# Performance work log

Hardware: AMD Instinct MI355X
Metric: run time of the kernel (lower is better)

## Reference

```python
import jax, jax.numpy as jnp
import numpy as np

B, S, MW = 128, 256, 21          # batch, sentence length, max word length
VOCAB, E_CHAR, E_WORD, K = 100, 50, 256, 5


def setup_inputs() -> dict:
    key = jax.random.key(0)
    ks = jax.random.split(key, 6)
    padded_sents = jax.random.randint(ks[0], (B, S, MW), 0, VOCAB)
    emb_table = jax.random.normal(ks[1], (VOCAB, E_CHAR), jnp.float32) * 0.1
    emb_table = emb_table.at[0].set(0.0)  # pad_token_idx row zeroed (padding_idx)
    conv_w = jax.random.normal(ks[2], (E_WORD, E_CHAR, K), jnp.float32) * 0.05
    conv_b = jnp.zeros((E_WORD,), jnp.float32)
    w_proj = jax.random.normal(ks[3], (E_WORD, E_WORD), jnp.float32) * 0.05
    b_proj = jnp.zeros((E_WORD,), jnp.float32)
    w_gate = jax.random.normal(ks[4], (E_WORD, E_WORD), jnp.float32) * 0.05
    b_gate = jnp.zeros((E_WORD,), jnp.float32)
    return {
        "padded_sents": padded_sents,
        "emb_table": emb_table,
        "conv_w": conv_w,
        "conv_b": conv_b,
        "w_proj": w_proj,
        "b_proj": b_proj,
        "w_gate": w_gate,
        "b_gate": b_gate,
    }


def reference(padded_sents, emb_table, conv_w, conv_b, w_proj, b_proj, w_gate, b_gate):
    b, s, mw = padded_sents.shape
    # char embedding lookup: [B,S,MW,E_CHAR]
    x = emb_table[padded_sents]
    # fold (B,S) into one batch dim and move channels first: [B*S, E_CHAR, MW]
    x = x.reshape(b * s, mw, -1).transpose(0, 2, 1)
    # Conv1d VALID over char positions: [B*S, E_WORD, MW-K+1]
    y = jax.lax.conv_general_dilated(
        x, conv_w, window_strides=(1,), padding="VALID",
        dimension_numbers=("NCH", "OIH", "NCH"))
    y = jax.nn.relu(y + conv_b[None, :, None])
    # max-pool over remaining char positions: [B*S, E_WORD]
    y = jnp.max(y, axis=2)
    # Highway network
    proj = jax.nn.relu(y @ w_proj.T + b_proj)
    gate = jax.nn.sigmoid(y @ w_gate.T + b_gate)
    out = gate * proj + (1.0 - gate) * y
    # dropout in eval mode (identity)
    return out.reshape(b, s, -1)
```

## Files before the change

### kernel.cpp

```cpp
#include <hip/hip_runtime.h>

#define B_     128
#define S_     256
#define MW_    21
#define VOCAB_ 100
#define EC_    50
#define EW_    256
#define KW_    5
#define T_     17
#define NW_    (B_ * S_)
#define GROWS  (VOCAB_ * KW_)
#define WPB    128
#define P1B    200

typedef _Float16 f16x8 __attribute__((ext_vector_type(8)));
typedef float    f32x4 __attribute__((ext_vector_type(4)));

__global__ __launch_bounds__(256) void k_prep(const float* __restrict__ emb,
                                              const float* __restrict__ cw,
                                              const float* __restrict__ Wp,
                                              const float* __restrict__ Wg,
                                              _Float16* __restrict__ g,
                                              _Float16* __restrict__ wpf,
                                              _Float16* __restrict__ wgf) {
  const int bi = blockIdx.x;
  if (bi < P1B) {
    __shared__ float ls[64 * 250];
    const int vp = bi >> 2, ot = bi & 3;
    const int o0 = ot * 64;
    const int tid = threadIdx.x;
    const float4* __restrict__ cw4 = (const float4*)cw + ot * 4000;
#pragma unroll 4
    for (int idx4 = tid; idx4 < 4000; idx4 += 256)
      *(float4*)&ls[idx4 * 4] = cw4[idx4];
    __syncthreads();

    const int l = tid & 63, wv = tid >> 6;
#pragma unroll
    for (int vv = 0; vv < 2; ++vv) {
      const int v = vp * 2 + vv;
      const float* __restrict__ er = emb + v * EC_;
      float acc = 0.f;
#pragma unroll
      for (int i = 0; i < EC_; ++i)
        acc += er[i] * ls[l * 250 + i * KW_ + wv];
      g[(v * KW_ + wv) * EW_ + o0 + l] = (_Float16)acc;
      if (wv == 0) {
        float a4 = 0.f;
#pragma unroll
        for (int i = 0; i < EC_; ++i)
          a4 += er[i] * ls[l * 250 + i * KW_ + 4];
        g[(v * KW_ + 4) * EW_ + o0 + l] = (_Float16)a4;
      }
    }
  } else {
    const int fl  = (bi - P1B) * 256 + threadIdx.x;
    const int nt  = fl >> 9;
    const int rem = fl & 511;
    const int ks  = rem >> 6;
    const int l   = rem & 63;
    const int n   = nt * 16 + (l & 15);
    const int kc  = ks * 32 + (l >> 4) * 8;
    const int src = n * EW_ + kc;
    const float4 p0 = *(const float4*)&Wp[src], p1 = *(const float4*)&Wp[src + 4];
    const float4 q0 = *(const float4*)&Wg[src], q1 = *(const float4*)&Wg[src + 4];
    f16x8 hp = {(_Float16)p0.x, (_Float16)p0.y, (_Float16)p0.z, (_Float16)p0.w,
                (_Float16)p1.x, (_Float16)p1.y, (_Float16)p1.z, (_Float16)p1.w};
    f16x8 hg = {(_Float16)q0.x, (_Float16)q0.y, (_Float16)q0.z, (_Float16)q0.w,
                (_Float16)q1.x, (_Float16)q1.y, (_Float16)q1.z, (_Float16)q1.w};
    *(f16x8*)&wpf[fl * 8] = hp;
    *(f16x8*)&wgf[fl * 8] = hg;
  }
}

__global__ __launch_bounds__(512, 2) void k_mega(const int* __restrict__ idx,
                                                 const _Float16* __restrict__ g,
                                                 const float* __restrict__ cb,
                                                 const _Float16* __restrict__ wpf,
                                                 const _Float16* __restrict__ wgf,
                                                 const float* __restrict__ bp,
                                                 const float* __restrict__ bg,
                                                 float* __restrict__ out) {
  __shared__ __align__(16) _Float16 lds[32768 + GROWS * 64];
  _Float16* y_s = lds;
  _Float16* g_s = lds + 32768;

  const int tid  = threadIdx.x;
  const int wave = tid >> 6, lane = tid & 63;
  const int m0 = blockIdx.x * WPB;
  const int wq = lane >> 3, og = lane & 7;

#pragma unroll
  for (int i = 0; i < 8; ++i) {
    const int c = tid + i * 512;
    if (c < GROWS * 8) {
      const int row = c >> 3, cc = c & 7;
      *(f16x8*)&g_s[row * 64 + cc * 8] = *(const f16x8*)&g[row * EW_ + cc * 8];
    }
  }
  __syncthreads();

  f16x8 pre[8];
#pragma unroll
  for (int chunk = 0; chunk < 4; ++chunk) {
    const int oc0 = chunk * 64;
    if (chunk < 3) {
#pragma unroll
      for (int i = 0; i < 8; ++i) {
        const int c = tid + i * 512;
        if (c < GROWS * 8) {
          const int row = c >> 3, cc = c & 7;
          pre[i] = *(const f16x8*)&g[row * EW_ + oc0 + 64 + cc * 8];
        }
      }
    }

    f16x8 bias;
#pragma unroll
    for (int j = 0; j < 8; ++j) bias[j] = (_Float16)cb[oc0 + og * 8 + j];

    const int ks_w    = chunk * 2 + (og >> 2);
    const int lane_hi = (og & 3) << 4;

#pragma unroll
    for (int it = 0; it < 2; ++it) {
      const int wl = it * 64 + wave * 8 + wq;
      const int* __restrict__ ip = idx + (m0 + wl) * MW_;
      int base[MW_];
#pragma unroll
      for (int c = 0; c < MW_; ++c)
        base[c] = ip[c] * (KW_ * 64) + og * 8;

      const _Float16 NEG = (_Float16)(-60000.0f);
      f16x8 mx = {NEG, NEG, NEG, NEG, NEG, NEG, NEG, NEG};
#pragma unroll
      for (int t = 0; t < T_; ++t) {
        f16x8 s = *(const f16x8*)&g_s[base[t]];
#pragma unroll
        for (int k = 1; k < KW_; ++k)
          s += *(const f16x8*)&g_s[base[t + k] + k * 64];
        mx = __builtin_elementwise_max(mx, s);
      }
      const f16x8 zero8 = {0, 0, 0, 0, 0, 0, 0, 0};
      mx = __builtin_elementwise_max(mx + bias, zero8);

      const int mt = wl >> 4;
      const int lt = ((wl & 15) | lane_hi) ^ og;
      *(f16x8*)&y_s[((mt * 8 + ks_w) * 64 + lt) * 8] = mx;
    }
    __syncthreads();
    if (chunk < 3) {
#pragma unroll
      for (int i = 0; i < 8; ++i) {
        const int c = tid + i * 512;
        if (c < GROWS * 8) {
          const int row = c >> 3, cc = c & 7;
          *(f16x8*)&g_s[row * 64 + cc * 8] = pre[i];
        }
      }
      __syncthreads();
    }
  }

  const int mtp2 = wave >> 2, nq = wave & 3;
  const int quad = lane >> 4, r16 = lane & 15;

  const f32x4 zero = {0.f, 0.f, 0.f, 0.f};
  f32x4 accp[4][4], accg[4][4];
#pragma unroll
  for (int mi = 0; mi < 4; ++mi)
#pragma unroll
    for (int nf = 0; nf < 4; ++nf) { accp[mi][nf] = zero; accg[mi][nf] = zero; }

#pragma unroll
  for (int ks = 0; ks < 8; ++ks) {
    const int key = ((ks & 1) << 2) | quad;
    f16x8 a[4];
#pragma unroll
    for (int mi = 0; mi < 4; ++mi)
      a[mi] = *(const f16x8*)&y_s[(((mtp2 * 4 + mi) * 8 + ks) * 64 + (lane ^ key)) * 8];
#pragma unroll
    for (int nf = 0; nf < 4; ++nf) {
      const int nt = nq * 4 + nf;
      const int off = ((nt * 8 + ks) * 64 + lane) * 8;
      const f16x8 bpv = *(const f16x8*)&wpf[off];
      const f16x8 bgv = *(const f16x8*)&wgf[off];
#pragma unroll
      for (int mi = 0; mi < 4; ++mi) {
        accp[mi][nf] = __builtin_amdgcn_mfma_f32_16x16x32_f16(a[mi], bpv, accp[mi][nf], 0, 0, 0);
        accg[mi][nf] = __builtin_amdgcn_mfma_f32_16x16x32_f16(a[mi], bgv, accg[mi][nf], 0, 0, 0);
      }
    }
  }

#pragma unroll
  for (int mi = 0; mi < 4; ++mi) {
    const int mt = mtp2 * 4 + mi;
#pragma unroll
    for (int nf = 0; nf < 4; ++nf) {
      const int n = nq * 64 + nf * 16 + r16;
      const float bpn = bp[n];
      const float bgn = bg[n];
      const int ks_e = n >> 5;
      const int lane_e = ((n >> 3) & 3) << 4;
      const int og_e = (n >> 3) & 7;
      const int je = n & 7;
#pragma unroll
      for (int reg = 0; reg < 4; ++reg) {
        const int m = mt * 16 + quad * 4 + reg;
        float p = fmaxf(accp[mi][nf][reg] + bpn, 0.f);
        const float gz = accg[mi][nf][reg] + bgn;
        const float gate = 1.f / (1.f + __expf(-gz));
        const float yv =
            (float)y_s[((mt * 8 + ks_e) * 64 + (((m & 15) | lane_e) ^ og_e)) * 8 + je];
        out[(m0 + m) * EW_ + n] = gate * p + (1.f - gate) * yv;
      }
    }
  }
}

extern "C" void kernel_launch(void* const* d_in, const int* in_sizes, int n_in,
                              void* d_out, int out_size, void* d_ws, size_t ws_size,
                              hipStream_t stream) {
  (void)in_sizes; (void)n_in; (void)out_size; (void)ws_size;
  const int*   idx = (const int*)d_in[0];
  const float* emb = (const float*)d_in[1];
  const float* cw  = (const float*)d_in[2];
  const float* cb  = (const float*)d_in[3];
  const float* wp  = (const float*)d_in[4];
  const float* bpp = (const float*)d_in[5];
  const float* wgt = (const float*)d_in[6];
  const float* bgg = (const float*)d_in[7];
  float* out = (float*)d_out;
  _Float16* g_ws = (_Float16*)d_ws;
  _Float16* wp_f = g_ws + GROWS * EW_;
  _Float16* wg_f = wp_f + EW_ * EW_;

  k_prep<<<P1B + 32, 256, 0, stream>>>(emb, cw, wp, wgt, g_ws, wp_f, wg_f);
  k_mega<<<NW_ / WPB, 512, 0, stream>>>(idx, g_ws, cb, wp_f, wg_f, bpp, bgg, out);
}
```

Baseline: 120.3 us.

## Warp-specialize mega kernel: conv waves overlap with MFMA highway waves per chunk

Halves words per block to 64 and splits the 8 waves into 4 conv waves and 4 GEMM waves. The GEMM waves consume each finished 64-channel chunk of y while the conv waves compute the next chunk, so the gather/max conv and the MFMA highway run concurrently instead of in sequence. Char index bases are hoisted into registers once per word. In exchange only half the waves do conv work, the block count doubles so the g table is reloaded twice as often, and register pressure in the specialized waves goes up.

```diff
diff --git a/kernel.cpp b/kernel.cpp
--- a/kernel.cpp
+++ b/kernel.cpp
@@ -10,7 +10,7 @@
 #define T_     17
 #define NW_    (B_ * S_)
 #define GROWS  (VOCAB_ * KW_)
-#define WPB    128
+#define WPB    64
 #define P1B    200
 
 typedef _Float16 f16x8 __attribute__((ext_vector_type(8)));
@@ -81,9 +81,9 @@
                                                  const float* __restrict__ bp,
                                                  const float* __restrict__ bg,
                                                  float* __restrict__ out) {
-  __shared__ __align__(16) _Float16 lds[32768 + GROWS * 64];
+  __shared__ __align__(16) _Float16 lds[16384 + GROWS * 64];
   _Float16* y_s = lds;
-  _Float16* g_s = lds + 32768;
+  _Float16* g_s = lds + 16384;
 
   const int tid  = threadIdx.x;
   const int wave = tid >> 6, lane = tid & 63;
@@ -100,6 +100,31 @@
   }
   __syncthreads();
 
+  const bool isConv = wave < 4;
+  const int quad = lane >> 4, r16 = lane & 15;
+  const int nq = wave & 3;
+
+  int base[2][MW_];
+  if (isConv) {
+#pragma unroll
+    for (int it = 0; it < 2; ++it) {
+      const int wl = it * 32 + wave * 8 + wq;
+      const int* __restrict__ ip = idx + (m0 + wl) * MW_;
+#pragma unroll
+      for (int c = 0; c < MW_; ++c)
+        base[it][c] = ip[c] * (KW_ * 64) + og * 8;
+    }
+  }
+
+  f32x4 accp[4][4], accg[4][4];
+  if (!isConv) {
+    const f32x4 zero = {0.f, 0.f, 0.f, 0.f};
+#pragma unroll
+    for (int mi = 0; mi < 4; ++mi)
+#pragma unroll
+      for (int nf = 0; nf < 4; ++nf) { accp[mi][nf] = zero; accg[mi][nf] = zero; }
+  }
+
   f16x8 pre[8];
 #pragma unroll
   for (int chunk = 0; chunk < 4; ++chunk) {
@@ -115,38 +140,53 @@
       }
     }
 
-    f16x8 bias;
-#pragma unroll
-    for (int j = 0; j < 8; ++j) bias[j] = (_Float16)cb[oc0 + og * 8 + j];
-
-    const int ks_w    = chunk * 2 + (og >> 2);
-    const int lane_hi = (og & 3) << 4;
-
-#pragma unroll
-    for (int it = 0; it < 2; ++it) {
-      const int wl = it * 64 + wave * 8 + wq;
-      const int* __restrict__ ip = idx + (m0 + wl) * MW_;
-      int base[MW_];
-#pragma unroll
-      for (int c = 0; c < MW_; ++c)
-        base[c] = ip[c] * (KW_ * 64) + og * 8;
-
-      const _Float16 NEG = (_Float16)(-60000.0f);
-      f16x8 mx = {NEG, NEG, NEG, NEG, NEG, NEG, NEG, NEG};
-#pragma unroll
-      for (int t = 0; t < T_; ++t) {
-        f16x8 s = *(const f16x8*)&g_s[base[t]];
-#pragma unroll
-        for (int k = 1; k < KW_; ++k)
-          s += *(const f16x8*)&g_s[base[t + k] + k * 64];
-        mx = __builtin_elementwise_max(mx, s);
-      }
-      const f16x8 zero8 = {0, 0, 0, 0, 0, 0, 0, 0};
-      mx = __builtin_elementwise_max(mx + bias, zero8);
-
-      const int mt = wl >> 4;
-      const int lt = ((wl & 15) | lane_hi) ^ og;
-      *(f16x8*)&y_s[((mt * 8 + ks_w) * 64 + lt) * 8] = mx;
+    if (isConv) {
+      f16x8 bias;
+#pragma unroll
+      for (int j = 0; j < 8; ++j) bias[j] = (_Float16)cb[oc0 + og * 8 + j];
+      const int ks_w    = chunk * 2 + (og >> 2);
+      const int lane_hi = (og & 3) << 4;
+#pragma unroll
+      for (int it = 0; it < 2; ++it) {
+        const int wl = it * 32 + wave * 8 + wq;
+        const _Float16 NEG = (_Float16)(-60000.0f);
+        f16x8 mx = {NEG, NEG, NEG, NEG, NEG, NEG, NEG, NEG};
+#pragma unroll
+        for (int t = 0; t < T_; ++t) {
+          f16x8 s = *(const f16x8*)&g_s[base[it][t]];
+#pragma unroll
+          for (int k = 1; k < KW_; ++k)
+            s += *(const f16x8*)&g_s[base[it][t + k] + k * 64];
+          mx = __builtin_elementwise_max(mx, s);
+        }
+        const f16x8 zero8 = {0, 0, 0, 0, 0, 0, 0, 0};
+        mx = __builtin_elementwise_max(mx + bias, zero8);
+        const int mt = wl >> 4;
+        const int lt = ((wl & 15) | lane_hi) ^ og;
+        *(f16x8*)&y_s[((mt * 8 + ks_w) * 64 + lt) * 8] = mx;
+      }
+    } else if (chunk > 0) {
+#pragma unroll
+      for (int ks2 = 0; ks2 < 2; ++ks2) {
+        const int ks = (chunk - 1) * 2 + ks2;
+        const int key = ((ks & 1) << 2) | quad;
+        f16x8 a[4];
+#pragma unroll
+        for (int mi = 0; mi < 4; ++mi)
+          a[mi] = *(const f16x8*)&y_s[((mi * 8 + ks) * 64 + (lane ^ key)) * 8];
+#pragma unroll
+        for (int nf = 0; nf < 4; ++nf) {
+          const int nt = nq * 4 + nf;
+          const int off = ((nt * 8 + ks) * 64 + lane) * 8;
+          const f16x8 bpv = *(const f16x8*)&wpf[off];
+          const f16x8 bgv = *(const f16x8*)&wgf[off];
+#pragma unroll
+          for (int mi = 0; mi < 4; ++mi) {
+            accp[mi][nf] = __builtin_amdgcn_mfma_f32_16x16x32_f16(a[mi], bpv, accp[mi][nf], 0, 0, 0);
+            accg[mi][nf] = __builtin_amdgcn_mfma_f32_16x16x32_f16(a[mi], bgv, accg[mi][nf], 0, 0, 0);
+          }
+        }
+      }
     }
     __syncthreads();
     if (chunk < 3) {
@@ -162,58 +202,50 @@
     }
   }
 
-  const int mtp2 = wave >> 2, nq = wave & 3;
-  const int quad = lane >> 4, r16 = lane & 15;
-
-  const f32x4 zero = {0.f, 0.f, 0.f, 0.f};
-  f32x4 accp[4][4], accg[4][4];
-#pragma unroll
-  for (int mi = 0; mi < 4; ++mi)
-#pragma unroll
-    for (int nf = 0; nf < 4; ++nf) { accp[mi][nf] = zero; accg[mi][nf] = zero; }
-
-#pragma unroll
-  for (int ks = 0; ks < 8; ++ks) {
-    const int key = ((ks & 1) << 2) | quad;
-    f16x8 a[4];
-#pragma unroll
-    for (int mi = 0; mi < 4; ++mi)
-      a[mi] = *(const f16x8*)&y_s[(((mtp2 * 4 + mi) * 8 + ks) * 64 + (lane ^ key)) * 8];
-#pragma unroll
-    for (int nf = 0; nf < 4; ++nf) {
-      const int nt = nq * 4 + nf;
-      const int off = ((nt * 8 + ks) * 64 + lane) * 8;
-      const f16x8 bpv = *(const f16x8*)&wpf[off];
-      const f16x8 bgv = *(const f16x8*)&wgf[off];
-#pragma unroll
-      for (int mi = 0; mi < 4; ++mi) {
-        accp[mi][nf] = __builtin_amdgcn_mfma_f32_16x16x32_f16(a[mi], bpv, accp[mi][nf], 0, 0, 0);
-        accg[mi][nf] = __builtin_amdgcn_mfma_f32_16x16x32_f16(a[mi], bgv, accg[mi][nf], 0, 0, 0);
-      }
-    }
-  }
-
-#pragma unroll
-  for (int mi = 0; mi < 4; ++mi) {
-    const int mt = mtp2 * 4 + mi;
-#pragma unroll
-    for (int nf = 0; nf < 4; ++nf) {
-      const int n = nq * 64 + nf * 16 + r16;
-      const float bpn = bp[n];
-      const float bgn = bg[n];
-      const int ks_e = n >> 5;
-      const int lane_e = ((n >> 3) & 3) << 4;
-      const int og_e = (n >> 3) & 7;
-      const int je = n & 7;
-#pragma unroll
-      for (int reg = 0; reg < 4; ++reg) {
-        const int m = mt * 16 + quad * 4 + reg;
-        float p = fmaxf(accp[mi][nf][reg] + bpn, 0.f);
-        const float gz = accg[mi][nf][reg] + bgn;
-        const float gate = 1.f / (1.f + __expf(-gz));
-        const float yv =
-            (float)y_s[((mt * 8 + ks_e) * 64 + (((m & 15) | lane_e) ^ og_e)) * 8 + je];
-        out[(m0 + m) * EW_ + n] = gate * p + (1.f - gate) * yv;
+  if (!isConv) {
+#pragma unroll
+    for (int ks2 = 0; ks2 < 2; ++ks2) {
+      const int ks = 6 + ks2;
+      const int key = ((ks & 1) << 2) | quad;
+      f16x8 a[4];
+#pragma unroll
+      for (int mi = 0; mi < 4; ++mi)
+        a[mi] = *(const f16x8*)&y_s[((mi * 8 + ks) * 64 + (lane ^ key)) * 8];
+#pragma unroll
+      for (int nf = 0; nf < 4; ++nf) {
+        const int nt = nq * 4 + nf;
+        const int off = ((nt * 8 + ks) * 64 + lane) * 8;
+        const f16x8 bpv = *(const f16x8*)&wpf[off];
+        const f16x8 bgv = *(const f16x8*)&wgf[off];
+#pragma unroll
+        for (int mi = 0; mi < 4; ++mi) {
+          accp[mi][nf] = __builtin_amdgcn_mfma_f32_16x16x32_f16(a[mi], bpv, accp[mi][nf], 0, 0, 0);
+          accg[mi][nf] = __builtin_amdgcn_mfma_f32_16x16x32_f16(a[mi], bgv, accg[mi][nf], 0, 0, 0);
+        }
+      }
+    }
+
+#pragma unroll
+    for (int mi = 0; mi < 4; ++mi) {
+#pragma unroll
+      for (int nf = 0; nf < 4; ++nf) {
+        const int n = nq * 64 + nf * 16 + r16;
+        const float bpn = bp[n];
+        const float bgn = bg[n];
+        const int ks_e = n >> 5;
+        const int lane_e = ((n >> 3) & 3) << 4;
+        const int og_e = (n >> 3) & 7;
+        const int je = n & 7;
+#pragma unroll
+        for (int reg = 0; reg < 4; ++reg) {
+          const int m = mi * 16 + quad * 4 + reg;
+          float p = fmaxf(accp[mi][nf][reg] + bpn, 0.f);
+          const float gz = accg[mi][nf][reg] + bgn;
+          const float gate = 1.f / (1.f + __expf(-gz));
+          const float yv =
+              (float)y_s[((mi * 8 + ks_e) * 64 + (((m & 15) | lane_e) ^ og_e)) * 8 + je];
+          out[(m0 + m) * EW_ + n] = gate * p + (1.f - gate) * yv;
+        }
       }
     }
   }
```

Result: slower. 155.4 us (+29.1%).

## Halve words per block and stream conv table in 32-channel chunks

Applied to the files above, without the earlier changes.

Blocks now handle 64 words with 256 threads instead of 128 words with 512 threads. The gathered conv table is staged through LDS in 32-channel slices over 8 chunks rather than 64-channel slices over 4, which roughly halves LDS per block and lets more blocks fit per CU. Each thread now keeps one word's character indices for the whole kernel instead of reloading them every chunk, and the y tile swizzle is changed to a rotation. The cost is twice as many chunk iterations and barriers per block, and every block re-reads the weight matrices for half as many rows.

```diff
diff --git a/kernel.cpp b/kernel.cpp
--- a/kernel.cpp
+++ b/kernel.cpp
@@ -10,7 +10,8 @@
 #define T_     17
 #define NW_    (B_ * S_)
 #define GROWS  (VOCAB_ * KW_)
-#define WPB    128
+#define WPB    64
+#define CCH    32
 #define P1B    200
 
 typedef _Float16 f16x8 __attribute__((ext_vector_type(8)));
@@ -73,7 +74,7 @@
   }
 }
 
-__global__ __launch_bounds__(512, 2) void k_mega(const int* __restrict__ idx,
+__global__ __launch_bounds__(256, 2) void k_mega(const int* __restrict__ idx,
                                                  const _Float16* __restrict__ g,
                                                  const float* __restrict__ cb,
                                                  const _Float16* __restrict__ wpf,
@@ -81,36 +82,45 @@
                                                  const float* __restrict__ bp,
                                                  const float* __restrict__ bg,
                                                  float* __restrict__ out) {
-  __shared__ __align__(16) _Float16 lds[32768 + GROWS * 64];
+  __shared__ __align__(16) _Float16 lds[16384 + GROWS * CCH];
   _Float16* y_s = lds;
-  _Float16* g_s = lds + 32768;
+  _Float16* g_s = lds + 16384;
 
   const int tid  = threadIdx.x;
   const int wave = tid >> 6, lane = tid & 63;
   const int m0 = blockIdx.x * WPB;
-  const int wq = lane >> 3, og = lane & 7;
+  const int w  = tid >> 2;
+  const int og = tid & 3;
 
 #pragma unroll
   for (int i = 0; i < 8; ++i) {
-    const int c = tid + i * 512;
-    if (c < GROWS * 8) {
-      const int row = c >> 3, cc = c & 7;
-      *(f16x8*)&g_s[row * 64 + cc * 8] = *(const f16x8*)&g[row * EW_ + cc * 8];
+    const int c = tid + i * 256;
+    if (c < GROWS * 4) {
+      const int row = c >> 2, cc = c & 3;
+      *(f16x8*)&g_s[row * CCH + cc * 8] = *(const f16x8*)&g[row * EW_ + cc * 8];
     }
   }
   __syncthreads();
 
+  const int* __restrict__ ipr = idx + (m0 + w) * MW_;
+  int base[MW_];
+#pragma unroll
+  for (int c = 0; c < MW_; ++c)
+    base[c] = ipr[c] * (KW_ * CCH) + og * 8;
+  const int mt_a = w >> 4;
+  const int lt   = (((w & 15) + 4 * og) & 15) | (og << 4);
+
   f16x8 pre[8];
 #pragma unroll
-  for (int chunk = 0; chunk < 4; ++chunk) {
-    const int oc0 = chunk * 64;
-    if (chunk < 3) {
+  for (int chunk = 0; chunk < 8; ++chunk) {
+    const int oc0 = chunk * CCH;
+    if (chunk < 7) {
 #pragma unroll
       for (int i = 0; i < 8; ++i) {
-        const int c = tid + i * 512;
-        if (c < GROWS * 8) {
-          const int row = c >> 3, cc = c & 7;
-          pre[i] = *(const f16x8*)&g[row * EW_ + oc0 + 64 + cc * 8];
+        const int c = tid + i * 256;
+        if (c < GROWS * 4) {
+          const int row = c >> 2, cc = c & 3;
+          pre[i] = *(const f16x8*)&g[row * EW_ + oc0 + CCH + cc * 8];
         }
       }
     }
@@ -119,51 +129,39 @@
 #pragma unroll
     for (int j = 0; j < 8; ++j) bias[j] = (_Float16)cb[oc0 + og * 8 + j];
 
-    const int ks_w    = chunk * 2 + (og >> 2);
-    const int lane_hi = (og & 3) << 4;
-
-#pragma unroll
-    for (int it = 0; it < 2; ++it) {
-      const int wl = it * 64 + wave * 8 + wq;
-      const int* __restrict__ ip = idx + (m0 + wl) * MW_;
-      int base[MW_];
-#pragma unroll
-      for (int c = 0; c < MW_; ++c)
-        base[c] = ip[c] * (KW_ * 64) + og * 8;
-
-      const _Float16 NEG = (_Float16)(-60000.0f);
-      f16x8 mx = {NEG, NEG, NEG, NEG, NEG, NEG, NEG, NEG};
-#pragma unroll
-      for (int t = 0; t < T_; ++t) {
-        f16x8 s = *(const f16x8*)&g_s[base[t]];
-#pragma unroll
-        for (int k = 1; k < KW_; ++k)
-          s += *(const f16x8*)&g_s[base[t + k] + k * 64];
-        mx = __builtin_elementwise_max(mx, s);
-      }
-      const f16x8 zero8 = {0, 0, 0, 0, 0, 0, 0, 0};
-      mx = __builtin_elementwise_max(mx + bias, zero8);
-
-      const int mt = wl >> 4;
-      const int lt = ((wl & 15) | lane_hi) ^ og;
-      *(f16x8*)&y_s[((mt * 8 + ks_w) * 64 + lt) * 8] = mx;
-    }
+    const _Float16 NEG = (_Float16)(-60000.0f);
+    f16x8 mx = {NEG, NEG, NEG, NEG, NEG, NEG, NEG, NEG};
+#pragma unroll
+    for (int t = 0; t < T_; ++t) {
+      f16x8 s = *(const f16x8*)&g_s[base[t]];
+#pragma unroll
+      for (int k = 1; k < KW_; ++k)
+        s += *(const f16x8*)&g_s[base[t + k] + k * CCH];
+      mx = __builtin_elementwise_max(mx, s);
+    }
+    const f16x8 zero8 = {0, 0, 0, 0, 0, 0, 0, 0};
+    mx = __builtin_elementwise_max(mx + bias, zero8);
+
+    *(f16x8*)&y_s[((mt_a * 8 + chunk) * 64 + lt) * 8] = mx;
+
     __syncthreads();
-    if (chunk < 3) {
+    if (chunk < 7) {
 #pragma unroll
       for (int i = 0; i < 8; ++i) {
-        const int c = tid + i * 512;
-        if (c < GROWS * 8) {
-          const int row = c >> 3, cc = c & 7;
-          *(f16x8*)&g_s[row * 64 + cc * 8] = pre[i];
+        const int c = tid + i * 256;
+        if (c < GROWS * 4) {
+          const int row = c >> 2, cc = c & 3;
+          *(f16x8*)&g_s[row * CCH + cc * 8] = pre[i];
         }
       }
       __syncthreads();
     }
   }
 
-  const int mtp2 = wave >> 2, nq = wave & 3;
+  const int nq = wave;
   const int quad = lane >> 4, r16 = lane & 15;
+  const int koct = lane >> 4;
+  const int ltr = (((lane & 15) + 4 * koct) & 15) | (koct << 4);
 
   const f32x4 zero = {0.f, 0.f, 0.f, 0.f};
   f32x4 accp[4][4], accg[4][4];
@@ -174,11 +172,10 @@
 
 #pragma unroll
   for (int ks = 0; ks < 8; ++ks) {
-    const int key = ((ks & 1) << 2) | quad;
     f16x8 a[4];
 #pragma unroll
     for (int mi = 0; mi < 4; ++mi)
-      a[mi] = *(const f16x8*)&y_s[(((mtp2 * 4 + mi) * 8 + ks) * 64 + (lane ^ key)) * 8];
+      a[mi] = *(const f16x8*)&y_s[((mi * 8 + ks) * 64 + ltr) * 8];
 #pragma unroll
     for (int nf = 0; nf < 4; ++nf) {
       const int nt = nq * 4 + nf;
@@ -195,24 +192,22 @@
 
 #pragma unroll
   for (int mi = 0; mi < 4; ++mi) {
-    const int mt = mtp2 * 4 + mi;
 #pragma unroll
     for (int nf = 0; nf < 4; ++nf) {
       const int n = nq * 64 + nf * 16 + r16;
       const float bpn = bp[n];
       const float bgn = bg[n];
       const int ks_e = n >> 5;
-      const int lane_e = ((n >> 3) & 3) << 4;
-      const int og_e = (n >> 3) & 7;
+      const int og_e = (n >> 3) & 3;
       const int je = n & 7;
 #pragma unroll
       for (int reg = 0; reg < 4; ++reg) {
-        const int m = mt * 16 + quad * 4 + reg;
+        const int m = mi * 16 + quad * 4 + reg;
+        const int lt_e = (((m & 15) + 4 * og_e) & 15) | (og_e << 4);
         float p = fmaxf(accp[mi][nf][reg] + bpn, 0.f);
         const float gz = accg[mi][nf][reg] + bgn;
         const float gate = 1.f / (1.f + __expf(-gz));
-        const float yv =
-            (float)y_s[((mt * 8 + ks_e) * 64 + (((m & 15) | lane_e) ^ og_e)) * 8 + je];
+        const float yv = (float)y_s[((mi * 8 + ks_e) * 64 + lt_e) * 8 + je];
         out[(m0 + m) * EW_ + n] = gate * p + (1.f - gate) * yv;
       }
     }
@@ -237,5 +232,5 @@
   _Float16* wg_f = wp_f + EW_ * EW_;
 
   k_prep<<<P1B + 32, 256, 0, stream>>>(emb, cw, wp, wgt, g_ws, wp_f, wg_f);
-  k_mega<<<NW_ / WPB, 512, 0, stream>>>(idx, g_ws, cb, wp_f, wg_f, bpp, bgg, out);
+  k_mega<<<NW_ / WPB, 256, 0, stream>>>(idx, g_ws, cb, wp_f, wg_f, bpp, bgg, out);
 }
```

Result: no change. 121.1 us (+0.6%).
